# Performance work log

Hardware: AMD Instinct MI355X
Metric: run time of the kernel (lower is better)

Reference implementation:

```python
import jax, jax.numpy as jnp
import numpy as np
import math

SI, VI = 128, 32
H_DIM = 32          # max(vi, vo) for q/k/v GVPs; max(vi, 0)=32 for weight_proj
HEADS = 4
N_ANCHORS = 32
S_H, V_H = SI // HEADS, VI // HEADS  # 32, 8


def _norm_no_nan(x, axis=-1, keepdims=False, eps=1e-8):
    return jnp.sqrt(jnp.maximum(jnp.sum(x * x, axis=axis, keepdims=keepdims), eps))


def _gvp_full(s, v, wh, ws_w, ws_b, wv, wsv_w, wsv_b):
    # GVP with activations=(silu, sigmoid), vector_gate=True, vo>0
    vt = jnp.swapaxes(v, -1, -2)                 # [..., 3, vi]
    vh = vt @ wh.T                               # [..., 3, h]
    vn = _norm_no_nan(vh, axis=-2)               # [..., h]
    s_out = jnp.concatenate([s, vn], -1) @ ws_w.T + ws_b   # [..., so]
    v_out = jnp.swapaxes(vh @ wv.T, -1, -2)      # [..., vo, 3]
    gate = jax.nn.sigmoid(s_out) @ wsv_w.T + wsv_b
    v_out = v_out * jax.nn.sigmoid(gate)[..., None]
    return jax.nn.silu(s_out), v_out


def _gvp_scalar(s, v, wh, ws_w, ws_b):
    # weight_proj: activations=(None, None), vo=0 -> scalar output only
    vt = jnp.swapaxes(v, -1, -2)
    vh = vt @ wh.T
    vn = _norm_no_nan(vh, axis=-2)
    return jnp.concatenate([s, vn], -1) @ ws_w.T + ws_b


def setup_inputs() -> dict:
    key = jax.random.key(0)
    ks = jax.random.split(key, 32)
    N, C = 8192, 16
    inp = {
        's': jax.random.normal(ks[0], (N, C, SI), jnp.float32),
        'v': jax.random.normal(ks[1], (N, C, VI, 3), jnp.float32),
    }

    def lin(k, out_d, in_d):
        return jax.random.normal(k, (out_d, in_d), jnp.float32) / math.sqrt(in_d)

    # weight_proj: GVP((128,32) -> (32,0)), h_dim = max(32,0) = 32
    inp['wp_wh'] = lin(ks[2], H_DIM, VI)
    inp['wp_ws_w'] = lin(ks[3], N_ANCHORS, H_DIM + SI)
    inp['wp_ws_b'] = jnp.zeros((N_ANCHORS,), jnp.float32)
    # to_q / to_k / to_v: GVP((128,32) -> (128,32)), h_dim = 32
    i = 4
    for p in ('q', 'k', 'vp'):
        inp[f'{p}_wh'] = lin(ks[i], H_DIM, VI); i += 1
        inp[f'{p}_ws_w'] = lin(ks[i], SI, H_DIM + SI); i += 1
        inp[f'{p}_ws_b'] = jnp.zeros((SI,), jnp.float32)
        inp[f'{p}_wv'] = lin(ks[i], VI, H_DIM); i += 1
        inp[f'{p}_wsv_w'] = lin(ks[i], VI, SI); i += 1
        inp[f'{p}_wsv_b'] = jnp.zeros((VI,), jnp.float32)
    return inp


def reference(s, v, wp_wh, wp_ws_w, wp_ws_b,
              q_wh, q_ws_w, q_ws_b, q_wv, q_wsv_w, q_wsv_b,
              k_wh, k_ws_w, k_ws_b, k_wv, k_wsv_w, k_wsv_b,
              vp_wh, vp_ws_w, vp_ws_b, vp_wv, vp_wsv_w, vp_wsv_b):
    N, C = s.shape[:2]
    H, r = HEADS, N_ANCHORS

    # Compress: softmax over nodes -> r anchors
    p_logits = _gvp_scalar(s, v, wp_wh, wp_ws_w, wp_ws_b)       # [N, C, r]
    p_weights = jax.nn.softmax(p_logits, axis=0)
    s_global = jnp.einsum('nca,ncs->acs', p_weights, s)          # [r, C, si]
    v_global = jnp.einsum('nca,ncvd->acvd', p_weights, v)        # [r, C, vi, 3]

    s_q, v_q = _gvp_full(s, v, q_wh, q_ws_w, q_ws_b, q_wv, q_wsv_w, q_wsv_b)
    s_k, v_k = _gvp_full(s_global, v_global, k_wh, k_ws_w, k_ws_b, k_wv, k_wsv_w, k_wsv_b)
    s_val, v_val = _gvp_full(s_global, v_global, vp_wh, vp_ws_w, vp_ws_b, vp_wv, vp_wsv_w, vp_wsv_b)

    # split heads
    qs = s_q.reshape(N, C, H, S_H); qv = v_q.reshape(N, C, H, V_H, 3)
    ks_ = s_k.reshape(r, C, H, S_H); kv = v_k.reshape(r, C, H, V_H, 3)
    vs = s_val.reshape(r, C, H, S_H); vv = v_val.reshape(r, C, H, V_H, 3)

    s_dot = jnp.einsum('nchs,rchs->nrch', qs, ks_)
    v_dot = jnp.einsum('nchvd,rchvd->nrch', qv, kv)
    energy = (s_dot + v_dot) / math.sqrt(S_H + V_H)
    alpha = jax.nn.softmax(energy, axis=1)                       # softmax over anchors r
    # dropout is identity at inference

    out_s = jnp.einsum('nrch,rchs->nchs', alpha, vs).reshape(N, C, SI)
    out_v = jnp.einsum('nrch,rchvd->nchvd', alpha, vv).reshape(N, C, VI, 3)
    return out_s, out_v
```

## Files before the change

kernel.cpp:

```cpp
#include <hip/hip_runtime.h>
#include <stdint.h>

typedef unsigned short ushort_t;
typedef __attribute__((ext_vector_type(8))) short short8;
typedef __attribute__((ext_vector_type(4))) float float4v;

static constexpr int N_=8192, C_=16;

static constexpr long OFF_LOGITS = 0;
static constexpr long OFF_PM  = 4194304;
static constexpr long OFF_PS  = 4210688;
static constexpr long OFF_M   = 4227072;
static constexpr long OFF_INV = 4227584;
static constexpr long OFF_SGL = 4228096;
static constexpr long OFF_VGL = 4293632;
static constexpr long OFF_KATT= 4342784;
static constexpr long OFF_VATT= 4408320;
static constexpr long OFF_WF  = 4473856;
static constexpr long WF_WHQ=0, WF_WHWP=1024, WF_KWH=2048, WF_KWS=3072, WF_KWV=23552,
  WF_KWSV=24576, WF_VWH=28672, WF_VWS=29696, WF_VWV=50176, WF_VWSV=51200,
  WF_B1=55296 , WF_BG=70656 ,
  WF_BV=72704 ;

static constexpr long VH_B   = 67108864;
static constexpr long AVN_B  = 92274688;
static constexpr long PART_B = 67108864;
static constexpr long PART_ROWSZ = 224;
static constexpr long PART_CHUNKSZ = 512*224;

__device__ __forceinline__ uint32_t f2bf(float f){
  uint32_t u = __float_as_uint(f);
  return (u + 0x7FFFu + ((u>>16)&1u)) >> 16;
}

__device__ __forceinline__ void split_bf(float f, short& hi, short& lo){
  uint32_t u = __float_as_uint(f);
  uint32_t h = (u + 0x7FFFu + ((u>>16)&1u)) >> 16;
  hi = (short)h;
  float fh = __uint_as_float(h << 16);
  float r = f - fh;
  uint32_t u2 = __float_as_uint(r);
  lo = (short)((u2 + 0x7FFFu + ((u2>>16)&1u)) >> 16);
}

__device__ __forceinline__ long katt_idx(int c, int h, int k, int r){
  int kt=k>>5, kk=k&31, nt=r>>4;
  int lane=((kk>>3)<<4)|(r&15), j=kk&7;
  return ((((long)(c*4+h)*2+kt)*2+nt)*64+lane)*8+j;
}
__device__ __forceinline__ long vatt_idx(int c, int h, int r, int n2){
  int nt=n2>>4;
  int lane=((r>>3)<<4)|(n2&15), j=r&7;
  return (((long)(c*4+h)*4+nt)*64+lane)*8+j;
}

__global__ void k0_prep(const float* __restrict__ wpwh, const float* __restrict__ wpws,
    const float* __restrict__ qwh, const float* __restrict__ qws, const float* __restrict__ qwv,
    const float* __restrict__ qwsv, const float* __restrict__ kwh, const float* __restrict__ kws,
    const float* __restrict__ kwv, const float* __restrict__ kwsv, const float* __restrict__ vwh,
    const float* __restrict__ vws, const float* __restrict__ vwv, const float* __restrict__ vwsv,
    float* __restrict__ wsf){
  int job=blockIdx.x, t=threadIdx.x;
  float* W = wsf + OFF_WF;
  auto tr=[&](const float* src, float* dst, int O, int J){
    for(int idx=t; idx<O*J; idx+=blockDim.x){int o=idx/J, j=idx-o*J; dst[j*O+o]=src[idx];}
  };
  switch(job){
    case 0: tr(qwh,  W+WF_WHQ, 32,32); break;
    case 1: tr(wpwh, W+WF_WHWP,32,32); break;
    case 2: tr(kwh,  W+WF_KWH, 32,32); break;
    case 3: tr(kws,  W+WF_KWS, 128,160); break;
    case 4: tr(kwv,  W+WF_KWV, 32,32); break;
    case 5: tr(kwsv, W+WF_KWSV,32,128); break;
    case 6: tr(vwh,  W+WF_VWH, 32,32); break;
    case 7: tr(vws,  W+WF_VWS, 128,160); break;
    case 8: tr(vwv,  W+WF_VWV, 32,32); break;
    case 9: tr(vwsv, W+WF_VWSV,32,128); break;
    case 10: {
      ushort_t* dst=(ushort_t*)(W+WF_B1);
      for(int idx=t; idx<30720; idx+=blockDim.x){
        int j=idx&7, lane=(idx>>3)&63, tn=idx>>9, nt=tn%10, kt=tn/10;
        int k=kt*32+((lane>>4)<<3)+j, n=nt*16+(lane&15);
        float val;
        if(k<128)       val = (n<128)? qws[n*160+k]            : wpws[(n-128)*160+k];
        else if(k<160)  val = (n<128)? qws[n*160+k]            : 0.f;
        else            val = (n<128)? 0.f                     : wpws[(n-128)*160+(k-32)];
        dst[idx]=(ushort_t)f2bf(val);
      } } break;
    case 11: {
      ushort_t* dst=(ushort_t*)(W+WF_BG);
      for(int idx=t; idx<4096; idx+=blockDim.x){
        int j=idx&7, lane=(idx>>3)&63, tn=idx>>9, nt=tn&1, kt=tn>>1;
        int k=kt*32+((lane>>4)<<3)+j, n=nt*16+(lane&15);
        dst[idx]=(ushort_t)f2bf(qwsv[n*128+k]);
      } } break;
    case 12: {
      ushort_t* dst=(ushort_t*)(W+WF_BV);
      for(int idx=t; idx<1024; idx+=blockDim.x){
        int j=idx&7, lane=(idx>>3)&63, nt=idx>>9;
        int k=((lane>>4)<<3)+j, n=nt*16+(lane&15);
        dst[idx]=(ushort_t)f2bf(qwv[n*32+k]);
      } } break;
  }
}

__global__ __launch_bounds__(256) void kA_vn(const float* __restrict__ v,
    const float* __restrict__ wsf, ushort_t* __restrict__ vh_s, ushort_t* __restrict__ avn_s){
  __shared__ float whq[1024], whwp[1024];
  __shared__ float vb[4][96];
  int t=threadIdx.x, wave=t>>6, lane=t&63;
  for(int i=t;i<1024;i+=256){ whq[i]=wsf[OFF_WF+WF_WHQ+i]; whwp[i]=wsf[OFF_WF+WF_WHWP+i]; }
  __syncthreads();
  int h=lane&31, half=lane>>5;
  for(int it=0; it<32; it++){
    long inst = ((long)blockIdx.x*4 + wave)*32 + it;
    if(lane<48) ((float2*)vb[wave])[lane] = ((const float2*)v)[inst*48+lane];
    float d0=0,d1=0,d2=0;
    for(int i=half*16;i<half*16+16;i++){ float w=whq[i*32+h];
      d0+=vb[wave][3*i]*w; d1+=vb[wave][3*i+1]*w; d2+=vb[wave][3*i+2]*w; }
    d0+=__shfl_xor(d0,32,64); d1+=__shfl_xor(d1,32,64); d2+=__shfl_xor(d2,32,64);
    if(lane<32){
      float vn=sqrtf(fmaxf(d0*d0+d1*d1+d2*d2,1e-8f));
      avn_s[inst*64+h]=(ushort_t)f2bf(vn);
      vh_s[(inst*3+0)*32+h]=(ushort_t)f2bf(d0);
      vh_s[(inst*3+1)*32+h]=(ushort_t)f2bf(d1);
      vh_s[(inst*3+2)*32+h]=(ushort_t)f2bf(d2);
    }
    float e0=0,e1=0,e2=0;
    for(int i=half*16;i<half*16+16;i++){ float w=whwp[i*32+h];
      e0+=vb[wave][3*i]*w; e1+=vb[wave][3*i+1]*w; e2+=vb[wave][3*i+2]*w; }
    e0+=__shfl_xor(e0,32,64); e1+=__shfl_xor(e1,32,64); e2+=__shfl_xor(e2,32,64);
    if(lane<32){
      float vn=sqrtf(fmaxf(e0*e0+e1*e1+e2*e2,1e-8f));
      avn_s[inst*64+32+h]=(ushort_t)f2bf(vn);
    }
  }
}

__global__ __launch_bounds__(256) void kB_gemm(const float* __restrict__ s,
    float* __restrict__ wsf,
    const float* __restrict__ qwsb, const float* __restrict__ wpwsb,
    const float* __restrict__ qwsvb,
    ushort_t* __restrict__ qatt, const ushort_t* __restrict__ vh_s,
    const ushort_t* __restrict__ avn_s){
  __shared__ ushort_t sigl[4][16*136];
  __shared__ float    gsigl[4][16*33];
  int t=threadIdx.x, wave=t>>6, lane=t&63;
  int l15=lane&15, lq=lane>>4;
  long m0 = ((long)blockIdx.x*4 + wave)*16;
  const short8* B1 = (const short8*)(wsf + OFF_WF + WF_B1);
  const short8* BG = (const short8*)(wsf + OFF_WF + WF_BG);
  const short8* BV = (const short8*)(wsf + OFF_WF + WF_BV);

  float4 f[4][2];
  #pragma unroll
  for(int kt=0;kt<4;kt++){
    const float* sp = s + (m0+l15)*128 + kt*32 + lq*8;
    f[kt][0]=*(const float4*)sp; f[kt][1]=*(const float4*)(sp+4);
  }
  short8 A4 = *(const short8*)&avn_s[(m0+l15)*64 + lq*8];
  short8 A5 = *(const short8*)&avn_s[(m0+l15)*64 + 32 + lq*8];
  short8 av0 = *(const short8*)&vh_s[(m0*3 + 0*16 + l15)*32 + lq*8];
  short8 av1 = *(const short8*)&vh_s[(m0*3 + 1*16 + l15)*32 + lq*8];
  short8 av2 = *(const short8*)&vh_s[(m0*3 + 2*16 + l15)*32 + lq*8];

  short8 A[6];
  #pragma unroll
  for(int kt=0;kt<4;kt++){
    short8 a;
    a[0]=(short)f2bf(f[kt][0].x); a[1]=(short)f2bf(f[kt][0].y);
    a[2]=(short)f2bf(f[kt][0].z); a[3]=(short)f2bf(f[kt][0].w);
    a[4]=(short)f2bf(f[kt][1].x); a[5]=(short)f2bf(f[kt][1].y);
    a[6]=(short)f2bf(f[kt][1].z); a[7]=(short)f2bf(f[kt][1].w);
    A[kt]=a;
  }
  A[4]=A4; A[5]=A5;

  float4v acc[10];
  #pragma unroll
  for(int i=0;i<10;i++) acc[i]=(float4v){0.f,0.f,0.f,0.f};
  #pragma unroll
  for(int kt=0;kt<6;kt++){
    #pragma unroll
    for(int nt=0;nt<10;nt++)
      acc[nt]=__builtin_amdgcn_mfma_f32_16x16x32_bf16(A[kt], B1[(kt*10+nt)*64+lane], acc[nt],0,0,0);
  }
  ushort_t* sl = sigl[wave]; float* gl = gsigl[wave];
  #pragma unroll
  for(int nt=0;nt<8;nt++){
    float b = qwsb[nt*16+l15];
    #pragma unroll
    for(int reg=0;reg<4;reg++){
      float x = acc[nt][reg] + b;
      float sg = 1.f/(1.f+__expf(-x));
      int row = lq*4+reg, col=nt*16+l15;
      long inst = m0+row;
      qatt[(inst*4 + (col>>5))*64 + (col&31)] = (ushort_t)f2bf(x*sg);
      sl[row*136+col] = (ushort_t)f2bf(sg);
    }
  }
  #pragma unroll
  for(int nt=8;nt<10;nt++){
    float b = wpwsb[(nt-8)*16+l15];
    #pragma unroll
    for(int reg=0;reg<4;reg++){
      long inst=m0+lq*4+reg;
      wsf[OFF_LOGITS + inst*32 + (nt-8)*16+l15] = acc[nt][reg]+b;
    }
  }
  float4v g0=(float4v){0.f,0.f,0.f,0.f}, g1=g0;
  #pragma unroll
  for(int kt=0;kt<4;kt++){
    short8 a = *(const short8*)&sl[l15*136 + kt*32 + lq*8];
    g0=__builtin_amdgcn_mfma_f32_16x16x32_bf16(a, BG[(kt*2+0)*64+lane], g0,0,0,0);
    g1=__builtin_amdgcn_mfma_f32_16x16x32_bf16(a, BG[(kt*2+1)*64+lane], g1,0,0,0);
  }
  {
    float b0 = qwsvb[l15], b1 = qwsvb[16+l15];
    #pragma unroll
    for(int reg=0;reg<4;reg++){
      int row=lq*4+reg;
      gl[row*33 + l15]    = 1.f/(1.f+__expf(-(g0[reg]+b0)));
      gl[row*33 + 16+l15] = 1.f/(1.f+__expf(-(g1[reg]+b1)));
    }
  }
  #pragma unroll
  for(int tt=0;tt<3;tt++){
    short8 a = (tt==0)? av0 : (tt==1)? av1 : av2;
    float4v v0=(float4v){0.f,0.f,0.f,0.f}, v1=v0;
    v0=__builtin_amdgcn_mfma_f32_16x16x32_bf16(a, BV[0*64+lane], v0,0,0,0);
    v1=__builtin_amdgcn_mfma_f32_16x16x32_bf16(a, BV[1*64+lane], v1,0,0,0);
    #pragma unroll
    for(int nt2=0;nt2<2;nt2++){
      #pragma unroll
      for(int reg=0;reg<4;reg++){
        int lr = tt*16 + lq*4 + reg;
        int il = lr/3, d = lr - il*3;
        int o = nt2*16+l15;
        float val = (nt2? v1[reg] : v0[reg]) * gl[il*33+o];
        long inst = m0 + il;
        qatt[(inst*4 + (o>>3))*64 + 32 + (o&7)*3 + d] = (ushort_t)f2bf(val);
      }
    }
  }
}

__global__ __launch_bounds__(256) void k2a_stats(float* __restrict__ ws){
  int c = blockIdx.x; int chunk = blockIdx.y;
  int t=threadIdx.x; int i=t>>5, a=t&31;
  const float* L = ws + OFF_LOGITS;
  float m=-1e30f, sum=0.f;
  for(int k2=0;k2<32;k2++){
    int n = chunk*256 + k2*8 + i;
    float x = L[((long)n*16 + c)*32 + a];
    float mn = fmaxf(m,x);
    sum = sum*__expf(m-mn) + __expf(x-mn);
    m = mn;
  }
  __shared__ float sm[8][32], ss[8][32];
  sm[i][a]=m; ss[i][a]=sum;
  __syncthreads();
  if(t<32){
    float M=sm[0][t], S=ss[0][t];
    for(int q=1;q<8;q++){
      float mq=sm[q][t], sq_=ss[q][t];
      float mn=fmaxf(M,mq); S=S*__expf(M-mn)+sq_*__expf(mq-mn); M=mn;
    }
    ws[OFF_PM + (chunk*16+c)*32 + t]=M;
    ws[OFF_PS + (chunk*16+c)*32 + t]=S;
  }
}

__global__ __launch_bounds__(256) void k2b_merge(float* __restrict__ ws){
  int t = blockIdx.x*256 + threadIdx.x;
  if(t>=512) return;
  int c=t>>5, a=t&31;
  float M=-1e30f, S=0.f;
  for(int ch=0; ch<32; ch++){
    float mq=ws[OFF_PM+(ch*16+c)*32+a], sq_=ws[OFF_PS+(ch*16+c)*32+a];
    float mn=fmaxf(M,mq); S=S*__expf(M-mn)+sq_*__expf(mq-mn); M=mn;
  }
  ws[OFF_M + t]=M; ws[OFF_INV + t]=1.0f/S;
}

template<int NMT, bool ISV>
__device__ __forceinline__ void k3_body(const float* __restrict__ X, int dx0, int pb0,
    const float* __restrict__ L, float M0, float M1, float I0, float I1,
    int c, int nb0, int l15, int lq, float* __restrict__ partc){
  constexpr int XP = ISV ? 96 : 128;
  float4v acc[NMT][2];
  #pragma unroll
  for(int mi=0;mi<NMT;mi++){
    acc[mi][0]=(float4v){0.f,0.f,0.f,0.f};
    acc[mi][1]=(float4v){0.f,0.f,0.f,0.f};
  }
  #pragma unroll
  for(int kt=0;kt<4;kt++){
    int nb = nb0 + kt*32 + lq*8;
    short8 bh0, bl0, bh1, bl1;
    #pragma unroll
    for(int j=0;j<8;j++){
      long ro = ((long)(nb+j)*16 + c)*32;
      float w0 = __expf(L[ro + l15]      - M0) * I0;
      float w1 = __expf(L[ro + 16 + l15] - M1) * I1;
      short h_, lo_;
      split_bf(w0, h_, lo_); bh0[j]=h_; bl0[j]=lo_;
      split_bf(w1, h_, lo_); bh1[j]=h_; bl1[j]=lo_;
    }
    #pragma unroll
    for(int mi=0;mi<NMT;mi++){
      short8 ah, al_;
      #pragma unroll
      for(int j=0;j<8;j++){
        float f = X[((long)(nb+j)*16 + c)*XP + dx0 + mi*16 + l15];
        short h_, lo_;
        split_bf(f, h_, lo_); ah[j]=h_; al_[j]=lo_;
      }
      acc[mi][0]=__builtin_amdgcn_mfma_f32_16x16x32_bf16(ah,  bh0, acc[mi][0],0,0,0);
      acc[mi][0]=__builtin_amdgcn_mfma_f32_16x16x32_bf16(al_, bh0, acc[mi][0],0,0,0);
      acc[mi][0]=__builtin_amdgcn_mfma_f32_16x16x32_bf16(ah,  bl0, acc[mi][0],0,0,0);
      acc[mi][1]=__builtin_amdgcn_mfma_f32_16x16x32_bf16(ah,  bh1, acc[mi][1],0,0,0);
      acc[mi][1]=__builtin_amdgcn_mfma_f32_16x16x32_bf16(al_, bh1, acc[mi][1],0,0,0);
      acc[mi][1]=__builtin_amdgcn_mfma_f32_16x16x32_bf16(ah,  bl1, acc[mi][1],0,0,0);
    }
  }
  #pragma unroll
  for(int mi=0;mi<NMT;mi++){
    #pragma unroll
    for(int nt=0;nt<2;nt++){
      int a = nt*16 + l15;
      long row = (long)(a*16 + c);
      float4 val = make_float4(acc[mi][nt][0], acc[mi][nt][1], acc[mi][nt][2], acc[mi][nt][3]);
      *(float4*)&partc[row*PART_ROWSZ + pb0 + mi*16 + lq*4] = val;
    }
  }
}

__global__ __launch_bounds__(256) void k3_globals(const float* __restrict__ s,
    const float* __restrict__ v, const float* __restrict__ ws, float* __restrict__ part){
  int c = blockIdx.x & 15; int chunk = blockIdx.x >> 4;
  int t=threadIdx.x, wave=t>>6, lane=t&63;
  int l15=lane&15, lq=lane>>4;
  const float* L = ws + OFF_LOGITS;
  float M0 = ws[OFF_M   + c*32 + l15],      M1 = ws[OFF_M   + c*32 + 16 + l15];
  float I0 = ws[OFF_INV + c*32 + l15],      I1 = ws[OFF_INV + c*32 + 16 + l15];
  int nb0 = chunk*128;
  float* partc = part + (long)chunk*PART_CHUNKSZ;
  if(wave==0)      k3_body<4,false>(s, 0,  0,   L, M0,M1,I0,I1, c, nb0, l15, lq, partc);
  else if(wave==1) k3_body<4,false>(s, 64, 64,  L, M0,M1,I0,I1, c, nb0, l15, lq, partc);
  else if(wave==2) k3_body<3,true >(v, 0,  128, L, M0,M1,I0,I1, c, nb0, l15, lq, partc);
  else             k3_body<3,true >(v, 48, 176, L, M0,M1,I0,I1, c, nb0, l15, lq, partc);
}

__global__ __launch_bounds__(64) void k4_kvgvp(float* __restrict__ wsf,
    const float* __restrict__ part,
    const float* __restrict__ k_wsb, const float* __restrict__ k_wsvb,
    const float* __restrict__ v_wsb, const float* __restrict__ v_wsvb){
  int a = blockIdx.x >> 4, c = blockIdx.x & 15;
  int lane = threadIdx.x;
  __shared__ __align__(16) float cat[160];
  __shared__ __align__(16) float vb2[96];
  __shared__ float vhb[96];
  __shared__ __align__(16) float sg[128];
  const float* W = wsf + OFF_WF;
  ushort_t* katt = (ushort_t*)(wsf + OFF_KATT);
  ushort_t* vatt = (ushort_t*)(wsf + OFF_VATT);
  long row = (long)a*16 + c;
  {
    float4 accp = make_float4(0.f,0.f,0.f,0.f);
    if(lane<56){
      const float* pp = part + row*PART_ROWSZ + lane*4;
      #pragma unroll 8
      for(int ch=0; ch<64; ch++){
        float4 x = *(const float4*)(pp + (long)ch*PART_CHUNKSZ);
        accp.x+=x.x; accp.y+=x.y; accp.z+=x.z; accp.w+=x.w;
      }
    }
    if(lane<32)      *(float4*)&cat[lane*4]      = accp;
    else if(lane<56) *(float4*)&vb2[(lane-32)*4] = accp;
  }
  __syncthreads();
  if(a==0){
    for(int idx=lane; idx<1024; idx+=64){
      int h2=idx&3, kk=56+((idx>>2)&7), r=idx>>5;
      katt[katt_idx(c,h2,kk,r)]=0;
      vatt[vatt_idx(c,h2,r,kk)]=0;
    }
  }
  int h = lane&31, half = lane>>5;
  for(int p=0;p<2;p++){
    const float* wht  = W + (p? WF_VWH  : WF_KWH);
    const float* wst  = W + (p? WF_VWS  : WF_KWS);
    const float* wvt  = W + (p? WF_VWV  : WF_KWV);
    const float* wsvt = W + (p? WF_VWSV : WF_KWSV);
    const float* bs   = p? v_wsb : k_wsb;
    const float* bsv  = p? v_wsvb : k_wsvb;
    float d0=0.f,d1=0.f,d2=0.f;
    for(int i=half*16; i<half*16+16; i++){
      float w_=wht[i*32+h];
      d0+=vb2[3*i]*w_; d1+=vb2[3*i+1]*w_; d2+=vb2[3*i+2]*w_;
    }
    d0 += __shfl_xor(d0,32,64); d1 += __shfl_xor(d1,32,64); d2 += __shfl_xor(d2,32,64);
    if(lane<32){
      cat[128+h] = sqrtf(fmaxf(d0*d0+d1*d1+d2*d2, 1e-8f));
      vhb[3*h]=d0; vhb[3*h+1]=d1; vhb[3*h+2]=d2;
    }
    __syncthreads();
    float a0=bs[lane], a1=bs[lane+64];
    for(int j=0;j<160;j+=4){
      float4 c4=*((float4*)&cat[j]);
      a0 += c4.x*wst[j*128+lane]      + c4.y*wst[(j+1)*128+lane]
          + c4.z*wst[(j+2)*128+lane]  + c4.w*wst[(j+3)*128+lane];
      a1 += c4.x*wst[j*128+64+lane]   + c4.y*wst[(j+1)*128+64+lane]
          + c4.z*wst[(j+2)*128+64+lane]+ c4.w*wst[(j+3)*128+64+lane];
    }
    float sig0=1.f/(1.f+__expf(-a0)), sig1=1.f/(1.f+__expf(-a1));
    float silu0=a0*sig0, silu1=a1*sig1;
    sg[lane]=sig0; sg[lane+64]=sig1;
    {
      int o=lane, hh2=o>>5, k=o&31;
      if(p==0) katt[katt_idx(c,hh2,k,a)] = (ushort_t)f2bf(silu0);
      else     vatt[vatt_idx(c,hh2,a,k)] = (ushort_t)f2bf(silu0);
    }
    {
      int o=lane+64, hh2=o>>5, k=o&31;
      if(p==0) katt[katt_idx(c,hh2,k,a)] = (ushort_t)f2bf(silu1);
      else     vatt[vatt_idx(c,hh2,a,k)] = (ushort_t)f2bf(silu1);
    }
    __syncthreads();
    float gacc=0.f;
    for(int o=half*64; o<half*64+64; o+=4){
      float4 s4_=*((float4*)&sg[o]);
      gacc += s4_.x*wsvt[o*32+h]+s4_.y*wsvt[(o+1)*32+h]+s4_.z*wsvt[(o+2)*32+h]+s4_.w*wsvt[(o+3)*32+h];
    }
    gacc += __shfl_xor(gacc,32,64);
    float sgate = 1.f/(1.f+__expf(-(gacc + bsv[h])));
    float e0=0.f,e1=0.f,e2=0.f;
    for(int hh=half*16; hh<half*16+16; hh++){
      float w_=wvt[hh*32+h];
      e0+=vhb[3*hh]*w_; e1+=vhb[3*hh+1]*w_; e2+=vhb[3*hh+2]*w_;
    }
    e0+=__shfl_xor(e0,32,64); e1+=__shfl_xor(e1,32,64); e2+=__shfl_xor(e2,32,64);
    if(lane<32){
      int hh2=lane>>3, oo=lane&7;
      float vals[3]={e0*sgate, e1*sgate, e2*sgate};
      #pragma unroll
      for(int d=0;d<3;d++){
        if(p==0) katt[katt_idx(c,hh2,32+oo*3+d,a)] = (ushort_t)f2bf(vals[d]);
        else     vatt[vatt_idx(c,hh2,a,32+oo*3+d)] = (ushort_t)f2bf(vals[d]);
      }
    }
    __syncthreads();
  }
}

__global__ __launch_bounds__(256) void k5_attn(const float* __restrict__ wsf, float* out){
  __shared__ ushort_t al[4][4*16*40];
  int t=threadIdx.x, wave=t>>6, lane=t&63;
  int l15=lane&15, lq=lane>>4;
  int c=blockIdx.y;
  long n0 = ((long)blockIdx.x*4+wave)*16;
  const ushort_t* qatt = (const ushort_t*)out;
  const short8* KA = (const short8*)(wsf + OFF_KATT);
  const short8* VA = (const short8*)(wsf + OFF_VATT);
  const float scale = 0.15811388300841897f;
  float4v e[4][2];
  #pragma unroll
  for(int h=0;h<4;h++){ e[h][0]=(float4v){0.f,0.f,0.f,0.f}; e[h][1]=e[h][0]; }
  #pragma unroll
  for(int h=0;h<4;h++){
    #pragma unroll
    for(int kt=0;kt<2;kt++){
      short8 a = *(const short8*)&qatt[(((n0+l15)*16 + c)*4 + h)*64 + kt*32 + lq*8];
      e[h][0]=__builtin_amdgcn_mfma_f32_16x16x32_bf16(a, KA[(((c*4+h)*2+kt)*2+0)*64+lane], e[h][0],0,0,0);
      e[h][1]=__builtin_amdgcn_mfma_f32_16x16x32_bf16(a, KA[(((c*4+h)*2+kt)*2+1)*64+lane], e[h][1],0,0,0);
    }
  }
  ushort_t* alw = al[wave];
  #pragma unroll
  for(int h=0;h<4;h++){
    #pragma unroll
    for(int reg=0;reg<4;reg++){
      float a0=e[h][0][reg]*scale, a1=e[h][1][reg]*scale;
      float m=fmaxf(a0,a1);
      m=fmaxf(m,__shfl_xor(m,1,64)); m=fmaxf(m,__shfl_xor(m,2,64));
      m=fmaxf(m,__shfl_xor(m,4,64)); m=fmaxf(m,__shfl_xor(m,8,64));
      float p0=__expf(a0-m), p1=__expf(a1-m);
      float sum=p0+p1;
      sum+=__shfl_xor(sum,1,64); sum+=__shfl_xor(sum,2,64);
      sum+=__shfl_xor(sum,4,64); sum+=__shfl_xor(sum,8,64);
      float inv=1.f/sum;
      int row=lq*4+reg;
      alw[h*640 + row*40 + l15]      = (ushort_t)f2bf(p0*inv);
      alw[h*640 + row*40 + 16 + l15] = (ushort_t)f2bf(p1*inv);
    }
  }
  float* outv = out + 16777216;
  #pragma unroll
  for(int h=0;h<4;h++){
    short8 a = *(const short8*)&alw[h*640 + l15*40 + lq*8];
    #pragma unroll
    for(int nt=0;nt<4;nt++){
      float4v o_=(float4v){0.f,0.f,0.f,0.f};
      o_=__builtin_amdgcn_mfma_f32_16x16x32_bf16(a, VA[((c*4+h)*4+nt)*64+lane], o_,0,0,0);
      #pragma unroll
      for(int reg=0;reg<4;reg++){
        int n2=nt*16+l15, row=lq*4+reg;
        long inst=(n0+row)*16+c;
        float val=o_[reg];
        if(n2<32)      out[inst*128 + h*32+n2]=val;
        else if(n2<56) outv[inst*96 + h*24 + n2-32]=val;
      }
    }
  }
}

extern "C" void kernel_launch(void* const* d_in, const int* in_sizes, int n_in,
                              void* d_out, int out_size, void* d_ws, size_t ws_size,
                              hipStream_t stream){
  (void)in_sizes; (void)n_in; (void)out_size; (void)ws_size;
  const float* s = (const float*)d_in[0];
  const float* v = (const float*)d_in[1];
  float* wsf = (float*)d_ws;
  float* out = (float*)d_out;
  ushort_t* qatt  = (ushort_t*)d_out;
  ushort_t* vh_s  = (ushort_t*)((char*)d_out + VH_B);
  ushort_t* avn_s = (ushort_t*)((char*)d_out + AVN_B);
  float* part = (float*)((char*)d_out + PART_B);
  k0_prep<<<13,256,0,stream>>>(
      (const float*)d_in[2],(const float*)d_in[3],
      (const float*)d_in[5],(const float*)d_in[6],(const float*)d_in[8],(const float*)d_in[9],
      (const float*)d_in[11],(const float*)d_in[12],(const float*)d_in[14],(const float*)d_in[15],
      (const float*)d_in[17],(const float*)d_in[18],(const float*)d_in[20],(const float*)d_in[21], wsf);
  kA_vn<<<1024,256,0,stream>>>(v, wsf, vh_s, avn_s);
  kB_gemm<<<2048,256,0,stream>>>(s, wsf, (const float*)d_in[7], (const float*)d_in[4],
                                 (const float*)d_in[10], qatt, vh_s, avn_s);
  k2a_stats<<<dim3(16,32),256,0,stream>>>(wsf);
  k2b_merge<<<2,256,0,stream>>>(wsf);
  k3_globals<<<1024,256,0,stream>>>(s, v, wsf, part);
  k4_kvgvp<<<512,64,0,stream>>>(wsf, part, (const float*)d_in[13], (const float*)d_in[16],
                                (const float*)d_in[19], (const float*)d_in[22]);
  k5_attn<<<dim3(128,16),256,0,stream>>>(wsf, out);
}
```

Baseline: 502.2 us.

## Stage q-attention output in LDS for coalesced stores, fold softmax merge into k3

kB_gemm now writes its bf16 scalar and gated-vector q outputs into a per-wave LDS tile and copies it out with coalesced 16-byte stores, where before it did scattered 2-byte global writes. Blocks shrink to 128 threads (two waves) with twice as many blocks, which keeps LDS per block in bounds. The separate k2b_merge launch is removed. Its 32-chunk max/sum merge is recomputed at the start of every k3_globals block, which adds redundant global reads and a syncthreads in exchange for one fewer launch.

```diff
diff --git a/kernel.cpp b/kernel.cpp
--- a/kernel.cpp
+++ b/kernel.cpp
@@ -137,17 +137,18 @@
   }
 }
 
-__global__ __launch_bounds__(256) void kB_gemm(const float* __restrict__ s,
+__global__ __launch_bounds__(128) void kB_gemm(const float* __restrict__ s,
     float* __restrict__ wsf,
     const float* __restrict__ qwsb, const float* __restrict__ wpwsb,
     const float* __restrict__ qwsvb,
     ushort_t* __restrict__ qatt, const ushort_t* __restrict__ vh_s,
     const ushort_t* __restrict__ avn_s){
-  __shared__ ushort_t sigl[4][16*136];
-  __shared__ float    gsigl[4][16*33];
+  __shared__ ushort_t sigl[2][16*136];
+  __shared__ float    gsigl[2][16*33];
+  __shared__ __align__(16) ushort_t qtile[2][16*264];
   int t=threadIdx.x, wave=t>>6, lane=t&63;
   int l15=lane&15, lq=lane>>4;
-  long m0 = ((long)blockIdx.x*4 + wave)*16;
+  long m0 = ((long)blockIdx.x*2 + wave)*16;
   const short8* B1 = (const short8*)(wsf + OFF_WF + WF_B1);
   const short8* BG = (const short8*)(wsf + OFF_WF + WF_BG);
   const short8* BV = (const short8*)(wsf + OFF_WF + WF_BV);
@@ -186,6 +187,11 @@
       acc[nt]=__builtin_amdgcn_mfma_f32_16x16x32_bf16(A[kt], B1[(kt*10+nt)*64+lane], acc[nt],0,0,0);
   }
   ushort_t* sl = sigl[wave]; float* gl = gsigl[wave];
+  ushort_t* qt = qtile[wave];
+  {
+    short8 z = {0,0,0,0,0,0,0,0};
+    *(short8*)&qt[l15*264 + lq*64 + 56] = z;
+  }
   #pragma unroll
   for(int nt=0;nt<8;nt++){
     float b = qwsb[nt*16+l15];
@@ -194,8 +200,7 @@
       float x = acc[nt][reg] + b;
       float sg = 1.f/(1.f+__expf(-x));
       int row = lq*4+reg, col=nt*16+l15;
-      long inst = m0+row;
-      qatt[(inst*4 + (col>>5))*64 + (col&31)] = (ushort_t)f2bf(x*sg);
+      qt[row*264 + (col>>5)*64 + (col&31)] = (ushort_t)f2bf(x*sg);
       sl[row*136+col] = (ushort_t)f2bf(sg);
     }
   }
@@ -238,10 +243,17 @@
         int il = lr/3, d = lr - il*3;
         int o = nt2*16+l15;
         float val = (nt2? v1[reg] : v0[reg]) * gl[il*33+o];
-        long inst = m0 + il;
-        qatt[(inst*4 + (o>>3))*64 + 32 + (o&7)*3 + d] = (ushort_t)f2bf(val);
+        qt[il*264 + (o>>3)*64 + 32 + (o&7)*3 + d] = (ushort_t)f2bf(val);
       }
     }
+  }
+  ushort_t* qdst = qatt + m0*256;
+  #pragma unroll
+  for(int ii=0; ii<8; ii++){
+    int idx = ii*512 + lane*8;
+    int row = idx>>8, off = idx&255;
+    short8 val = *(const short8*)&qt[row*264+off];
+    *(short8*)&qdst[idx] = val;
   }
 }
 
@@ -269,18 +281,6 @@
     ws[OFF_PM + (chunk*16+c)*32 + t]=M;
     ws[OFF_PS + (chunk*16+c)*32 + t]=S;
   }
-}
-
-__global__ __launch_bounds__(256) void k2b_merge(float* __restrict__ ws){
-  int t = blockIdx.x*256 + threadIdx.x;
-  if(t>=512) return;
-  int c=t>>5, a=t&31;
-  float M=-1e30f, S=0.f;
-  for(int ch=0; ch<32; ch++){
-    float mq=ws[OFF_PM+(ch*16+c)*32+a], sq_=ws[OFF_PS+(ch*16+c)*32+a];
-    float mn=fmaxf(M,mq); S=S*__expf(M-mn)+sq_*__expf(mq-mn); M=mn;
-  }
-  ws[OFF_M + t]=M; ws[OFF_INV + t]=1.0f/S;
 }
 
 template<int NMT, bool ISV>
@@ -342,8 +342,20 @@
   int t=threadIdx.x, wave=t>>6, lane=t&63;
   int l15=lane&15, lq=lane>>4;
   const float* L = ws + OFF_LOGITS;
-  float M0 = ws[OFF_M   + c*32 + l15],      M1 = ws[OFF_M   + c*32 + 16 + l15];
-  float I0 = ws[OFF_INV + c*32 + l15],      I1 = ws[OFF_INV + c*32 + 16 + l15];
+  __shared__ float sM[32], sI[32];
+  if(t<32){
+    int a=t;
+    float M=-1e30f, S=0.f;
+    #pragma unroll 4
+    for(int ch=0; ch<32; ch++){
+      float mq=ws[OFF_PM+(ch*16+c)*32+a], sq_=ws[OFF_PS+(ch*16+c)*32+a];
+      float mn=fmaxf(M,mq); S=S*__expf(M-mn)+sq_*__expf(mq-mn); M=mn;
+    }
+    sM[a]=M; sI[a]=1.0f/S;
+  }
+  __syncthreads();
+  float M0 = sM[l15], M1 = sM[16+l15];
+  float I0 = sI[l15], I1 = sI[16+l15];
   int nb0 = chunk*128;
   float* partc = part + (long)chunk*PART_CHUNKSZ;
   if(wave==0)      k3_body<4,false>(s, 0,  0,   L, M0,M1,I0,I1, c, nb0, l15, lq, partc);
@@ -533,10 +545,9 @@
       (const float*)d_in[11],(const float*)d_in[12],(const float*)d_in[14],(const float*)d_in[15],
       (const float*)d_in[17],(const float*)d_in[18],(const float*)d_in[20],(const float*)d_in[21], wsf);
   kA_vn<<<1024,256,0,stream>>>(v, wsf, vh_s, avn_s);
-  kB_gemm<<<2048,256,0,stream>>>(s, wsf, (const float*)d_in[7], (const float*)d_in[4],
+  kB_gemm<<<4096,128,0,stream>>>(s, wsf, (const float*)d_in[7], (const float*)d_in[4],
                                  (const float*)d_in[10], qatt, vh_s, avn_s);
   k2a_stats<<<dim3(16,32),256,0,stream>>>(wsf);
-  k2b_merge<<<2,256,0,stream>>>(wsf);
   k3_globals<<<1024,256,0,stream>>>(s, v, wsf, part);
   k4_kvgvp<<<512,64,0,stream>>>(wsf, part, (const float*)d_in[13], (const float*)d_in[16],
                                 (const float*)d_in[19], (const float*)d_in[22]);
```

Measured after the change: 568.2 us. 1.13x slower.
